# Kernel tuning notes

Hardware: AMD Instinct MI355X
Metric: run time of the kernel (lower is better)

Reference implementation:

```python
import jax, jax.numpy as jnp
import numpy as np

L_F, D_F = 32, 16      # fast window / hop
L_S, D_S = 32, 16      # slow window / hop
H = 32                 # SSM hidden dim
GH = 64                # GRU hidden dim
N_GRU = 4


def setup_inputs() -> dict:
    key = jax.random.key(0)
    ks = jax.random.split(key, 16)
    B, T = 2, 64000
    s = 0.1
    return {
        "x": jax.random.normal(ks[0], (B, T), jnp.float32),
        # slow branch input FC (1 -> GH), stored as (in, out)
        "slow_in_W": jax.random.normal(ks[1], (1, GH), jnp.float32) * s,
        "slow_in_b": jax.random.normal(ks[2], (GH,), jnp.float32) * s,
        # 4 stacked GRU layers, torch gate order [r, z, n], stored (in, 3*GH)
        "gru_Wih": jax.random.normal(ks[3], (N_GRU, GH, 3 * GH), jnp.float32) * s,
        "gru_Whh": jax.random.normal(ks[4], (N_GRU, GH, 3 * GH), jnp.float32) * s,
        "gru_bih": jax.random.normal(ks[5], (N_GRU, 3 * GH), jnp.float32) * s,
        "gru_bhh": jax.random.normal(ks[6], (N_GRU, 3 * GH), jnp.float32) * s,
        # slow branch output FC (GH -> GH)
        "slow_out_W": jax.random.normal(ks[7], (GH, GH), jnp.float32) * s,
        "slow_out_b": jax.random.normal(ks[8], (GH,), jnp.float32) * s,
        # slow_to_ssm (GH -> 2H)
        "s2s_W": jax.random.normal(ks[9], (GH, 2 * H), jnp.float32) * s,
        "s2s_b": jax.random.normal(ks[10], (2 * H,), jnp.float32) * s,
        # fast branch F_IN (1 -> H) and F_OUT (H -> 1)
        "fin_W": jax.random.normal(ks[11], (1, H), jnp.float32) * s,
        "fin_b": jax.random.normal(ks[12], (H,), jnp.float32) * s,
        "fout_W": jax.random.normal(ks[13], (H, 1), jnp.float32) * s,
        "fout_b": jax.random.normal(ks[14], (1,), jnp.float32) * s,
    }


def _forward(x, slow_in_W, slow_in_b, gru_Wih, gru_Whh, gru_bih, gru_bhh,
             slow_out_W, slow_out_b, s2s_W, s2s_b, fin_W, fin_b, fout_W, fout_b):
    B, T = x.shape
    nf = (T - L_F) // D_F + 1   # fast frame count
    ns = (T - L_S) // D_S + 1   # slow frame count
    fidx = jnp.arange(nf)[:, None] * D_F + jnp.arange(L_F)[None, :]  # (nf, L_F)
    sidx = jnp.arange(ns)[:, None] * D_S + jnp.arange(L_S)[None, :]  # (ns, L_S)
    frames = x[:, fidx]                                  # (B, nf, L_F)  == x.unfold

    BS = B * ns
    xs = x[:, sidx].reshape(BS, L_S, 1)
    h = jax.nn.relu(xs @ slow_in_W + slow_in_b)          # (BS, L_S, GH)
    for l in range(N_GRU):
        Whh, bhh = gru_Whh[l], gru_bhh[l]
        xg = h @ gru_Wih[l] + gru_bih[l]                 # (BS, L_S, 3GH)

        def step(hc, xg_t, Whh=Whh, bhh=bhh):
            hg = hc @ Whh + bhh
            r = jax.nn.sigmoid(xg_t[:, :GH] + hg[:, :GH])
            z = jax.nn.sigmoid(xg_t[:, GH:2 * GH] + hg[:, GH:2 * GH])
            n = jnp.tanh(xg_t[:, 2 * GH:] + r * hg[:, 2 * GH:])
            hn = (1.0 - z) * n + z * hc
            return hn, hn

        _, seq = jax.lax.scan(step, jnp.zeros((BS, GH), x.dtype), jnp.swapaxes(xg, 0, 1))
        h = jax.nn.relu(jnp.swapaxes(seq, 0, 1))         # (BS, L_S, GH)
    slow_feat = h[:, -1, :] @ slow_out_W + slow_out_b    # (BS, GH)

    # ---- modulation parameters ----
    eps = (slow_feat @ s2s_W + s2s_b).reshape(B, ns, 2 * H)
    A_s = jax.nn.sigmoid(eps[..., :H])                   # (B, ns, H)
    g_s = eps[..., H:]
    delta = D_S // D_F
    A_flat = jnp.repeat(A_s, delta, axis=1)[:, :nf].reshape(B * nf, H)
    g_flat = jnp.repeat(g_s, delta, axis=1)[:, :nf].reshape(B * nf, H)

    # ---- fast branch: diagonal SSM h_t = A*h_{t-1} + g * F_IN(x_t) ----
    ff = frames.reshape(B * nf, L_F, 1)
    x_emb = (ff @ fin_W + fin_b) * g_flat[:, None, :]    # (B*nf, L_F, H)

    def ssm_step(hc, xt):
        hn = A_flat * hc + xt
        return hn, hn

    _, hall = jax.lax.scan(ssm_step, jnp.zeros((B * nf, H), x.dtype),
                           jnp.swapaxes(x_emb, 0, 1))
    hall = jnp.swapaxes(hall, 0, 1)                      # (B*nf, L_F, H)
    s_hat = (hall @ fout_W + fout_b)[..., 0].reshape(B, nf, L_F)

    # ---- overlap-add (F.fold) ----
    out = jnp.zeros((B, T), x.dtype).at[:, fidx].add(s_hat)
    return out


def reference(x, slow_in_W, slow_in_b, gru_Wih, gru_Whh, gru_bih, gru_bhh,
              slow_out_W, slow_out_b, s2s_W, s2s_b, fin_W, fin_b, fout_W, fout_b):
    return _forward(x, slow_in_W, slow_in_b, gru_Wih, gru_Whh, gru_bih, gru_bhh,
                    slow_out_W, slow_out_b, s2s_W, s2s_b, fin_W, fin_b, fout_W, fout_b)
```

## Files before the change

kernel.cpp:

```cpp
#include <hip/hip_runtime.h>

#define GH 64
#define LS 32
#define HF 32
#define DS 16

#define NLOG2E -1.4426950408889634f
#define P2LOG2E 2.8853900817779268f

typedef short bf16x8 __attribute__((ext_vector_type(8)));
typedef float f32x4 __attribute__((ext_vector_type(4)));

#define MFMA16(a, b, c) __builtin_amdgcn_mfma_f32_16x16x32_bf16(a, b, c, 0, 0, 0)

__device__ __forceinline__ unsigned int f2bf_rne(float f) {
    unsigned int u = __float_as_uint(f);
    return (u + 0x7FFFu + ((u >> 16) & 1u)) >> 16;
}
__device__ __forceinline__ unsigned short f2bf_h(float f) {
    return (unsigned short)((__float_as_uint(f) + 0x8000u) >> 16);
}
__device__ __forceinline__ unsigned int pack_trunc(float v0, float v1) {
    return __builtin_amdgcn_perm(__float_as_uint(v1), __float_as_uint(v0),
                                 0x07060302u);
}
__device__ __forceinline__ bf16x8 as_frag(uint4 u) {
    union { uint4 a; bf16x8 b; } cv; cv.a = u; return cv.b;
}

__device__ __forceinline__ bf16x8 ld_afrag(const unsigned short* slot, int m,
                                           int quad, int half) {
    int b   = half * 4 + quad;
    int idx = (m << 6) + ((b ^ (m & 7)) << 3);
    return as_frag(*reinterpret_cast<const uint4*>(slot + idx));
}

__global__ __launch_bounds__(256) void prep_weights(
    const float* __restrict__ Wih, const float* __restrict__ Whh,
    const float* __restrict__ soW, const float* __restrict__ s2sW,
    unsigned short* __restrict__ wsW)
{
    int idx = blockIdx.x * 256 + threadIdx.x;
    if (idx >= 104 * 1024) return;
    int j = idx & 7, lane = (idx >> 3) & 63, kc = (idx >> 9) & 1, rest = idx >> 10;
    int k = kc * 32 + ((lane >> 4) << 3) + j;
    int c = lane & 15;
    float v;
    if (rest < 96) {
        int jt = rest & 3, mt = rest >> 2;
        int l = mt / 6, mat = mt - l * 6;
        int col = jt * 16 + c;
        const float* W = (mat < 3) ? Wih + (size_t)l * GH * 192
                                   : Whh + (size_t)l * GH * 192;
        int m3 = (mat < 3) ? mat : mat - 3;
        v = W[k * 192 + m3 * 64 + col];
        v *= (m3 == 2) ? P2LOG2E : NLOG2E;
    } else {
        int r2 = rest - 96;
        int jt = r2 & 3, m2 = r2 >> 2;
        int col = jt * 16 + c;
        v = (m2 ? s2sW : soW)[k * 64 + col];
        if (m2 && jt < 2) v *= NLOG2E;
    }
    wsW[idx] = (unsigned short)f2bf_rne(v);
}

__global__ __launch_bounds__(256, 2) void slowfast_fused(
    const float* __restrict__ x,
    const float* __restrict__ siW,  const float* __restrict__ sib,
    const float* __restrict__ bih,  const float* __restrict__ bhh,
    const float* __restrict__ sob,  const float* __restrict__ s2sb,
    const float* __restrict__ finW, const float* __restrict__ finb,
    const float* __restrict__ foutW, const float* __restrict__ foutb,
    const unsigned short* __restrict__ wsW,
    float* __restrict__ out,
    int T, int ns, int BS)
{
    __shared__ __align__(16) unsigned short hseq[LS * 16 * 64];
    __shared__ __align__(16) unsigned short hrec[2 * 16 * 64];
    __shared__ float xs[16 * 33];
    __shared__ float AG[16 * 65];

    const int tid  = threadIdx.x;
    const int lane = tid & 63;
    const int jt   = tid >> 6;
    const int c    = lane & 15;
    const int quad = lane >> 4;
    const int col  = jt * 16 + c;
    const int seqbase = blockIdx.x * 16;
    const uint4* wf = reinterpret_cast<const uint4*>(wsW);

    for (int p = tid; p < 512; p += 256) {
        int seq = p >> 5, t = p & 31;
        int q = seqbase + seq; if (q > BS - 1) q = BS - 1;
        int b  = (q >= ns) ? 1 : 0;
        int si = q - b * ns;
        xs[seq * 33 + t] = x[b * T + si * DS + t];
    }
    __syncthreads();

    {
        int chp = tid & 31;
        int grp = tid >> 5;
        int ch  = chp << 1;
        float w0 = siW[ch], w1 = siW[ch + 1];
        float b0 = sib[ch], b1 = sib[ch + 1];
        #pragma unroll 4
        for (int it = 0; it < 64; ++it) {
            int p = grp + (it << 3);
            int s = p >> 5, t = p & 31;
            float xv = xs[s * 33 + t];
            float v0 = fmaxf(fmaf(xv, w0, b0), 0.0f);
            float v1 = fmaxf(fmaf(xv, w1, b1), 0.0f);
            int idx = (t << 10) + (s << 6) + ((((ch >> 3) ^ (s & 7))) << 3) + (ch & 7);
            *reinterpret_cast<unsigned int*>(&hseq[idx]) = pack_trunc(v0, v1);
        }
    }

    int wIdx[4];
    #pragma unroll
    for (int i = 0; i < 4; ++i) {
        int row = quad * 4 + i;
        wIdx[i] = (row << 6) + ((((col >> 3) ^ (row & 7))) << 3) + (col & 7);
    }

    __syncthreads();

    bf16x8 a0 = ld_afrag(hseq, c, quad, 0);
    bf16x8 a1 = ld_afrag(hseq, c, quad, 1);

    for (int l = 0; l < 4; ++l) {
        bf16x8 BiR[2], BiZ[2], BiN[2], BhR[2], BhZ[2], BhN[2];
        #pragma unroll
        for (int kc = 0; kc < 2; ++kc) {
            int base = (l * 6 * 4 + jt) * 128 + kc * 64 + lane;
            BiR[kc] = as_frag(wf[base]);
            BiZ[kc] = as_frag(wf[base + 512]);
            BiN[kc] = as_frag(wf[base + 1024]);
            BhR[kc] = as_frag(wf[base + 1536]);
            BhZ[kc] = as_frag(wf[base + 2048]);
            BhN[kc] = as_frag(wf[base + 2560]);
        }
        float bRs  = NLOG2E  * (bih[l * 192 + col]      + bhh[l * 192 + col]);
        float bZs  = NLOG2E  * (bih[l * 192 + 64 + col] + bhh[l * 192 + 64 + col]);
        float bNIs = P2LOG2E * bih[l * 192 + 128 + col];
        float bNHs = P2LOG2E * bhh[l * 192 + 128 + col];
        const f32x4 vbR  = (f32x4){bRs,  bRs,  bRs,  bRs};
        const f32x4 vbZ  = (f32x4){bZs,  bZs,  bZs,  bZs};
        const f32x4 vbNI = (f32x4){bNIs, bNIs, bNIs, bNIs};
        const f32x4 vbNH = (f32x4){bNHs, bNHs, bNHs, bNHs};

        float hprev[4] = {0.0f, 0.0f, 0.0f, 0.0f};

        #pragma unroll 2
        for (int t = 0; t < LS; ++t) {
            f32x4 aR  = MFMA16(a0, BiR[0], vbR);
            f32x4 aZ  = MFMA16(a0, BiZ[0], vbZ);
            f32x4 aNI = MFMA16(a0, BiN[0], vbNI);
            aR  = MFMA16(a1, BiR[1], aR);
            aZ  = MFMA16(a1, BiZ[1], aZ);
            aNI = MFMA16(a1, BiN[1], aNI);
            f32x4 aNH = vbNH;
            if (t > 0) {
                const unsigned short* hb = hrec + (((t - 1) & 1) << 10);
                bf16x8 h0 = ld_afrag(hb, c, quad, 0);
                bf16x8 h1 = ld_afrag(hb, c, quad, 1);
                aR  = MFMA16(h0, BhR[0], aR);
                aZ  = MFMA16(h0, BhZ[0], aZ);
                aNH = MFMA16(h0, BhN[0], aNH);
                aR  = MFMA16(h1, BhR[1], aR);
                aZ  = MFMA16(h1, BhZ[1], aZ);
                aNH = MFMA16(h1, BhN[1], aNH);
            }
            unsigned short* wb = hseq + (t << 10);
            unsigned short* wr = hrec + ((t & 1) << 10);
            #pragma unroll
            for (int i = 0; i < 4; ++i) {
                float r  = __builtin_amdgcn_rcpf(1.0f + __builtin_amdgcn_exp2f(aR[i]));
                float z  = __builtin_amdgcn_rcpf(1.0f + __builtin_amdgcn_exp2f(aZ[i]));
                float e  = __builtin_amdgcn_exp2f(fmaf(r, aNH[i], aNI[i]));
                float n  = fmaf(-2.0f, __builtin_amdgcn_rcpf(e + 1.0f), 1.0f);
                float hn = fmaf(z, hprev[i] - n, n);
                hprev[i] = hn;
                wr[wIdx[i]] = f2bf_h(hn);
                wb[wIdx[i]] = f2bf_h(fmaxf(hn, 0.0f));
            }
            const unsigned short* nb = hseq + (((t + 1) & 31) << 10);
            a0 = ld_afrag(nb, c, quad, 0);
            a1 = ld_afrag(nb, c, quad, 1);
            __syncthreads();
        }
    }

    {
        bf16x8 e0 = ld_afrag(hseq + (31 << 10), c, quad, 0);
        bf16x8 e1 = ld_afrag(hseq + (31 << 10), c, quad, 1);
        bf16x8 Bso[2], Bs2[2];
        #pragma unroll
        for (int kc = 0; kc < 2; ++kc) {
            Bso[kc] = as_frag(wf[(96 + jt)  * 128 + kc * 64 + lane]);
            Bs2[kc] = as_frag(wf[(100 + jt) * 128 + kc * 64 + lane]);
        }
        float sb = sob[col];
        f32x4 accS = (f32x4){sb, sb, sb, sb};
        accS = MFMA16(e0, Bso[0], accS);
        accS = MFMA16(e1, Bso[1], accS);
        #pragma unroll
        for (int i = 0; i < 4; ++i)
            hseq[wIdx[i]] = f2bf_h(accS[i]);
        __syncthreads();
        bf16x8 s0 = ld_afrag(hseq, c, quad, 0);
        bf16x8 s1 = ld_afrag(hseq, c, quad, 1);
        float eb = (jt < 2) ? NLOG2E * s2sb[col] : s2sb[col];
        f32x4 accE = (f32x4){eb, eb, eb, eb};
        accE = MFMA16(s0, Bs2[0], accE);
        accE = MFMA16(s1, Bs2[1], accE);
        #pragma unroll
        for (int i = 0; i < 4; ++i) {
            int row = quad * 4 + i;
            float v = accE[i];
            AG[row * 65 + col] = (jt < 2)
                ? __builtin_amdgcn_rcpf(1.0f + __builtin_amdgcn_exp2f(v)) : v;
        }
    }
    __syncthreads();
    {
        int fch = tid & 31;
        float Gfw = finW[fch], Gbw = finb[fch], cFo = foutW[fch], cfb = foutb[0];
        #pragma unroll
        for (int half = 0; half < 2; ++half) {
            int frame = half * 8 + (tid >> 5);
            int q = seqbase + frame;
            if (q < BS) {
                int b  = (q >= ns) ? 1 : 0;
                int fi = q - b * ns;
                float cA = AG[frame * 65 + fch];
                float cG = AG[frame * 65 + 32 + fch];
                float Gf = Gfw * cG;
                float Gb = Gbw * cG;
                float h = 0.0f;
                const float* xrow = xs + frame * 33;
                float* op = out + (size_t)b * T + fi * DS;
                #pragma unroll 1
                for (int t = 0; t < LS; ++t) {
                    h = fmaf(cA, h, fmaf(xrow[t], Gf, Gb));
                    float s = h * cFo;
                    s += __shfl_xor(s, 1);
                    s += __shfl_xor(s, 2);
                    s += __shfl_xor(s, 4);
                    s += __shfl_xor(s, 8);
                    s += __shfl_xor(s, 16);
                    if (fch == 0) atomicAdd(&op[t], s + cfb);
                }
            }
        }
    }
}

extern "C" void kernel_launch(void* const* d_in, const int* in_sizes, int n_in,
                              void* d_out, int out_size, void* d_ws, size_t ws_size,
                              hipStream_t stream)
{
    (void)n_in; (void)ws_size;
    const float* x     = (const float*)d_in[0];
    const float* siW   = (const float*)d_in[1];
    const float* sib   = (const float*)d_in[2];
    const float* Wih   = (const float*)d_in[3];
    const float* Whh   = (const float*)d_in[4];
    const float* bih   = (const float*)d_in[5];
    const float* bhh   = (const float*)d_in[6];
    const float* soW   = (const float*)d_in[7];
    const float* sob   = (const float*)d_in[8];
    const float* s2sW  = (const float*)d_in[9];
    const float* s2sb  = (const float*)d_in[10];
    const float* finW  = (const float*)d_in[11];
    const float* finb  = (const float*)d_in[12];
    const float* foutW = (const float*)d_in[13];
    const float* foutb = (const float*)d_in[14];

    int T  = in_sizes[0] / 2;
    int ns = (T - LS) / DS + 1;
    int BS = 2 * ns;

    unsigned short* wsW = (unsigned short*)d_ws;

    (void)hipMemsetAsync(d_out, 0, (size_t)out_size * sizeof(float), stream);

    prep_weights<<<dim3(416), dim3(256), 0, stream>>>(Wih, Whh, soW, s2sW, wsW);

    slowfast_fused<<<dim3((BS + 15) / 16), dim3(256), 0, stream>>>(
        x, siW, sib, bih, bhh, sob, s2sb, finW, finb, foutW, foutb,
        wsW, (float*)d_out, T, ns, BS);
}
```

Baseline: 171.6 us.

## Wavefront-pipeline GRU layers across warps with two sequence groups per block

The block becomes 1024 threads, with each of 16 waves owning one GRU layer and one column tile. The four layers run as a diagonal wavefront over time steps, and layer outputs pass through small double-buffered LDS rings instead of a full 32-step sequence buffer. Each block handles two 16-sequence groups, so the MFMA chains of two groups interleave. Layer-0 inputs are now built in registers from x, and weights are loaded once per wave. This gives more parallel waves and overlap across layers, at the cost of three extra pipeline steps and a barrier every step across 1024 threads.

```diff
diff --git a/kernel.cpp b/kernel.cpp
--- a/kernel.cpp
+++ b/kernel.cpp
@@ -33,6 +33,27 @@
     int b   = half * 4 + quad;
     int idx = (m << 6) + ((b ^ (m & 7)) << 3);
     return as_frag(*reinterpret_cast<const uint4*>(slot + idx));
+}
+
+__device__ __forceinline__ bf16x8 build_l0(float xv, const float* w, const float* b) {
+    float4 w0 = reinterpret_cast<const float4*>(w)[0];
+    float4 w1 = reinterpret_cast<const float4*>(w)[1];
+    float4 b0 = reinterpret_cast<const float4*>(b)[0];
+    float4 b1 = reinterpret_cast<const float4*>(b)[1];
+    float v0 = fmaxf(fmaf(xv, w0.x, b0.x), 0.0f);
+    float v1 = fmaxf(fmaf(xv, w0.y, b0.y), 0.0f);
+    float v2 = fmaxf(fmaf(xv, w0.z, b0.z), 0.0f);
+    float v3 = fmaxf(fmaf(xv, w0.w, b0.w), 0.0f);
+    float v4 = fmaxf(fmaf(xv, w1.x, b1.x), 0.0f);
+    float v5 = fmaxf(fmaf(xv, w1.y, b1.y), 0.0f);
+    float v6 = fmaxf(fmaf(xv, w1.z, b1.z), 0.0f);
+    float v7 = fmaxf(fmaf(xv, w1.w, b1.w), 0.0f);
+    union { uint4 u; bf16x8 v; } cv;
+    cv.u.x = pack_trunc(v0, v1);
+    cv.u.y = pack_trunc(v2, v3);
+    cv.u.z = pack_trunc(v4, v5);
+    cv.u.w = pack_trunc(v6, v7);
+    return cv.v;
 }
 
 __global__ __launch_bounds__(256) void prep_weights(
@@ -65,7 +86,7 @@
     wsW[idx] = (unsigned short)f2bf_rne(v);
 }
 
-__global__ __launch_bounds__(256, 2) void slowfast_fused(
+__global__ __launch_bounds__(1024, 4) void slowfast_fused(
     const float* __restrict__ x,
     const float* __restrict__ siW,  const float* __restrict__ sib,
     const float* __restrict__ bih,  const float* __restrict__ bhh,
@@ -76,46 +97,52 @@
     float* __restrict__ out,
     int T, int ns, int BS)
 {
-    __shared__ __align__(16) unsigned short hseq[LS * 16 * 64];
-    __shared__ __align__(16) unsigned short hrec[2 * 16 * 64];
-    __shared__ float xs[16 * 33];
-    __shared__ float AG[16 * 65];
+    __shared__ __align__(16) unsigned short ring[2][3][2][1024];
+    __shared__ __align__(16) unsigned short hrec[2][4][2][1024];
+    __shared__ __align__(16) unsigned short h31[2][1024];
+    __shared__ float xs[2][16 * 33];
+    __shared__ float AG[2][16 * 65];
+    __shared__ float swb[128];
 
     const int tid  = threadIdx.x;
     const int lane = tid & 63;
-    const int jt   = tid >> 6;
+    const int wid  = tid >> 6;
+    const int l    = wid >> 2;
+    const int jt   = wid & 3;
     const int c    = lane & 15;
     const int quad = lane >> 4;
     const int col  = jt * 16 + c;
-    const int seqbase = blockIdx.x * 16;
+    const int seqbase = blockIdx.x * 32;
     const uint4* wf = reinterpret_cast<const uint4*>(wsW);
 
-    for (int p = tid; p < 512; p += 256) {
-        int seq = p >> 5, t = p & 31;
-        int q = seqbase + seq; if (q > BS - 1) q = BS - 1;
+    {
+        int s32 = tid >> 5, t = tid & 31;
+        int q = seqbase + s32; if (q > BS - 1) q = BS - 1;
         int b  = (q >= ns) ? 1 : 0;
         int si = q - b * ns;
-        xs[seq * 33 + t] = x[b * T + si * DS + t];
-    }
-    __syncthreads();
-
-    {
-        int chp = tid & 31;
-        int grp = tid >> 5;
-        int ch  = chp << 1;
-        float w0 = siW[ch], w1 = siW[ch + 1];
-        float b0 = sib[ch], b1 = sib[ch + 1];
-        #pragma unroll 4
-        for (int it = 0; it < 64; ++it) {
-            int p = grp + (it << 3);
-            int s = p >> 5, t = p & 31;
-            float xv = xs[s * 33 + t];
-            float v0 = fmaxf(fmaf(xv, w0, b0), 0.0f);
-            float v1 = fmaxf(fmaf(xv, w1, b1), 0.0f);
-            int idx = (t << 10) + (s << 6) + ((((ch >> 3) ^ (s & 7))) << 3) + (ch & 7);
-            *reinterpret_cast<unsigned int*>(&hseq[idx]) = pack_trunc(v0, v1);
-        }
-    }
+        xs[s32 >> 4][(s32 & 15) * 33 + t] = x[b * T + si * DS + t];
+    }
+    if (tid < 64) { swb[tid] = siW[tid]; swb[64 + tid] = sib[tid]; }
+
+    bf16x8 BiR[2], BiZ[2], BiN[2], BhR[2], BhZ[2], BhN[2];
+    #pragma unroll
+    for (int kc = 0; kc < 2; ++kc) {
+        int base = (l * 6 * 4 + jt) * 128 + kc * 64 + lane;
+        BiR[kc] = as_frag(wf[base]);
+        BiZ[kc] = as_frag(wf[base + 512]);
+        BiN[kc] = as_frag(wf[base + 1024]);
+        BhR[kc] = as_frag(wf[base + 1536]);
+        BhZ[kc] = as_frag(wf[base + 2048]);
+        BhN[kc] = as_frag(wf[base + 2560]);
+    }
+    float bRs  = NLOG2E  * (bih[l * 192 + col]      + bhh[l * 192 + col]);
+    float bZs  = NLOG2E  * (bih[l * 192 + 64 + col] + bhh[l * 192 + 64 + col]);
+    float bNIs = P2LOG2E * bih[l * 192 + 128 + col];
+    float bNHs = P2LOG2E * bhh[l * 192 + 128 + col];
+    const f32x4 vbR  = (f32x4){bRs,  bRs,  bRs,  bRs};
+    const f32x4 vbZ  = (f32x4){bZs,  bZs,  bZs,  bZs};
+    const f32x4 vbNI = (f32x4){bNIs, bNIs, bNIs, bNIs};
+    const f32x4 vbNH = (f32x4){bNHs, bNHs, bNHs, bNHs};
 
     int wIdx[4];
     #pragma unroll
@@ -124,93 +151,90 @@
         wIdx[i] = (row << 6) + ((((col >> 3) ^ (row & 7))) << 3) + (col & 7);
     }
 
+    float hprev[2][4] = {{0, 0, 0, 0}, {0, 0, 0, 0}};
+
     __syncthreads();
 
-    bf16x8 a0 = ld_afrag(hseq, c, quad, 0);
-    bf16x8 a1 = ld_afrag(hseq, c, quad, 1);
-
-    for (int l = 0; l < 4; ++l) {
-        bf16x8 BiR[2], BiZ[2], BiN[2], BhR[2], BhZ[2], BhN[2];
+    #pragma unroll 2
+    for (int tau = 0; tau < LS + 3; ++tau) {
+        int t = tau - l;
+        if (t >= 0 && t < LS) {
+            #pragma unroll
+            for (int grp = 0; grp < 2; ++grp) {
+                bf16x8 a0, a1;
+                if (l == 0) {
+                    float xv = xs[grp][c * 33 + t];
+                    a0 = build_l0(xv, &swb[quad * 8],      &swb[64 + quad * 8]);
+                    a1 = build_l0(xv, &swb[32 + quad * 8], &swb[96 + quad * 8]);
+                } else {
+                    const unsigned short* ab = ring[grp][l - 1][t & 1];
+                    a0 = ld_afrag(ab, c, quad, 0);
+                    a1 = ld_afrag(ab, c, quad, 1);
+                }
+                f32x4 aR  = MFMA16(a0, BiR[0], vbR);
+                f32x4 aZ  = MFMA16(a0, BiZ[0], vbZ);
+                f32x4 aNI = MFMA16(a0, BiN[0], vbNI);
+                aR  = MFMA16(a1, BiR[1], aR);
+                aZ  = MFMA16(a1, BiZ[1], aZ);
+                aNI = MFMA16(a1, BiN[1], aNI);
+                f32x4 aNH = vbNH;
+                if (t > 0) {
+                    const unsigned short* hb = hrec[grp][l][(t - 1) & 1];
+                    bf16x8 h0 = ld_afrag(hb, c, quad, 0);
+                    bf16x8 h1 = ld_afrag(hb, c, quad, 1);
+                    aR  = MFMA16(h0, BhR[0], aR);
+                    aZ  = MFMA16(h0, BhZ[0], aZ);
+                    aNH = MFMA16(h0, BhN[0], aNH);
+                    aR  = MFMA16(h1, BhR[1], aR);
+                    aZ  = MFMA16(h1, BhZ[1], aZ);
+                    aNH = MFMA16(h1, BhN[1], aNH);
+                }
+                unsigned short* wr = hrec[grp][l][t & 1];
+                unsigned short* wb = (l < 3) ? ring[grp][l][t & 1] : h31[grp];
+                bool wrelu = (l < 3) | (t == LS - 1);
+                #pragma unroll
+                for (int i = 0; i < 4; ++i) {
+                    float r  = __builtin_amdgcn_rcpf(1.0f + __builtin_amdgcn_exp2f(aR[i]));
+                    float z  = __builtin_amdgcn_rcpf(1.0f + __builtin_amdgcn_exp2f(aZ[i]));
+                    float e  = __builtin_amdgcn_exp2f(fmaf(r, aNH[i], aNI[i]));
+                    float n  = fmaf(-2.0f, __builtin_amdgcn_rcpf(e + 1.0f), 1.0f);
+                    float hn = fmaf(z, hprev[grp][i] - n, n);
+                    hprev[grp][i] = hn;
+                    wr[wIdx[i]] = f2bf_h(hn);
+                    if (wrelu)
+                        wb[wIdx[i]] = f2bf_h(fmaxf(hn, 0.0f));
+                }
+            }
+        }
+        __syncthreads();
+    }
+
+    if (wid < 8) {
+        int grp1 = l;
+        bf16x8 e0 = ld_afrag(h31[grp1], c, quad, 0);
+        bf16x8 e1 = ld_afrag(h31[grp1], c, quad, 1);
+        bf16x8 Bso[2];
         #pragma unroll
-        for (int kc = 0; kc < 2; ++kc) {
-            int base = (l * 6 * 4 + jt) * 128 + kc * 64 + lane;
-            BiR[kc] = as_frag(wf[base]);
-            BiZ[kc] = as_frag(wf[base + 512]);
-            BiN[kc] = as_frag(wf[base + 1024]);
-            BhR[kc] = as_frag(wf[base + 1536]);
-            BhZ[kc] = as_frag(wf[base + 2048]);
-            BhN[kc] = as_frag(wf[base + 2560]);
-        }
-        float bRs  = NLOG2E  * (bih[l * 192 + col]      + bhh[l * 192 + col]);
-        float bZs  = NLOG2E  * (bih[l * 192 + 64 + col] + bhh[l * 192 + 64 + col]);
-        float bNIs = P2LOG2E * bih[l * 192 + 128 + col];
-        float bNHs = P2LOG2E * bhh[l * 192 + 128 + col];
-        const f32x4 vbR  = (f32x4){bRs,  bRs,  bRs,  bRs};
-        const f32x4 vbZ  = (f32x4){bZs,  bZs,  bZs,  bZs};
-        const f32x4 vbNI = (f32x4){bNIs, bNIs, bNIs, bNIs};
-        const f32x4 vbNH = (f32x4){bNHs, bNHs, bNHs, bNHs};
-
-        float hprev[4] = {0.0f, 0.0f, 0.0f, 0.0f};
-
-        #pragma unroll 2
-        for (int t = 0; t < LS; ++t) {
-            f32x4 aR  = MFMA16(a0, BiR[0], vbR);
-            f32x4 aZ  = MFMA16(a0, BiZ[0], vbZ);
-            f32x4 aNI = MFMA16(a0, BiN[0], vbNI);
-            aR  = MFMA16(a1, BiR[1], aR);
-            aZ  = MFMA16(a1, BiZ[1], aZ);
-            aNI = MFMA16(a1, BiN[1], aNI);
-            f32x4 aNH = vbNH;
-            if (t > 0) {
-                const unsigned short* hb = hrec + (((t - 1) & 1) << 10);
-                bf16x8 h0 = ld_afrag(hb, c, quad, 0);
-                bf16x8 h1 = ld_afrag(hb, c, quad, 1);
-                aR  = MFMA16(h0, BhR[0], aR);
-                aZ  = MFMA16(h0, BhZ[0], aZ);
-                aNH = MFMA16(h0, BhN[0], aNH);
-                aR  = MFMA16(h1, BhR[1], aR);
-                aZ  = MFMA16(h1, BhZ[1], aZ);
-                aNH = MFMA16(h1, BhN[1], aNH);
-            }
-            unsigned short* wb = hseq + (t << 10);
-            unsigned short* wr = hrec + ((t & 1) << 10);
-            #pragma unroll
-            for (int i = 0; i < 4; ++i) {
-                float r  = __builtin_amdgcn_rcpf(1.0f + __builtin_amdgcn_exp2f(aR[i]));
-                float z  = __builtin_amdgcn_rcpf(1.0f + __builtin_amdgcn_exp2f(aZ[i]));
-                float e  = __builtin_amdgcn_exp2f(fmaf(r, aNH[i], aNI[i]));
-                float n  = fmaf(-2.0f, __builtin_amdgcn_rcpf(e + 1.0f), 1.0f);
-                float hn = fmaf(z, hprev[i] - n, n);
-                hprev[i] = hn;
-                wr[wIdx[i]] = f2bf_h(hn);
-                wb[wIdx[i]] = f2bf_h(fmaxf(hn, 0.0f));
-            }
-            const unsigned short* nb = hseq + (((t + 1) & 31) << 10);
-            a0 = ld_afrag(nb, c, quad, 0);
-            a1 = ld_afrag(nb, c, quad, 1);
-            __syncthreads();
-        }
-    }
-
-    {
-        bf16x8 e0 = ld_afrag(hseq + (31 << 10), c, quad, 0);
-        bf16x8 e1 = ld_afrag(hseq + (31 << 10), c, quad, 1);
-        bf16x8 Bso[2], Bs2[2];
-        #pragma unroll
-        for (int kc = 0; kc < 2; ++kc) {
-            Bso[kc] = as_frag(wf[(96 + jt)  * 128 + kc * 64 + lane]);
-            Bs2[kc] = as_frag(wf[(100 + jt) * 128 + kc * 64 + lane]);
-        }
+        for (int kc = 0; kc < 2; ++kc)
+            Bso[kc] = as_frag(wf[(96 + jt) * 128 + kc * 64 + lane]);
         float sb = sob[col];
         f32x4 accS = (f32x4){sb, sb, sb, sb};
         accS = MFMA16(e0, Bso[0], accS);
         accS = MFMA16(e1, Bso[1], accS);
+        unsigned short* sf = ring[grp1][0][0];
         #pragma unroll
         for (int i = 0; i < 4; ++i)
-            hseq[wIdx[i]] = f2bf_h(accS[i]);
-        __syncthreads();
-        bf16x8 s0 = ld_afrag(hseq, c, quad, 0);
-        bf16x8 s1 = ld_afrag(hseq, c, quad, 1);
+            sf[wIdx[i]] = f2bf_h(accS[i]);
+    }
+    __syncthreads();
+    if (wid >= 8) {
+        int grp2 = l - 2;
+        bf16x8 s0 = ld_afrag(ring[grp2][0][0], c, quad, 0);
+        bf16x8 s1 = ld_afrag(ring[grp2][0][0], c, quad, 1);
+        bf16x8 Bs2[2];
+        #pragma unroll
+        for (int kc = 0; kc < 2; ++kc)
+            Bs2[kc] = as_frag(wf[(100 + jt) * 128 + kc * 64 + lane]);
         float eb = (jt < 2) ? NLOG2E * s2sb[col] : s2sb[col];
         f32x4 accE = (f32x4){eb, eb, eb, eb};
         accE = MFMA16(s0, Bs2[0], accE);
@@ -219,39 +243,37 @@
         for (int i = 0; i < 4; ++i) {
             int row = quad * 4 + i;
             float v = accE[i];
-            AG[row * 65 + col] = (jt < 2)
+            AG[grp2][row * 65 + col] = (jt < 2)
                 ? __builtin_amdgcn_rcpf(1.0f + __builtin_amdgcn_exp2f(v)) : v;
         }
     }
     __syncthreads();
     {
-        int fch = tid & 31;
-        float Gfw = finW[fch], Gbw = finb[fch], cFo = foutW[fch], cfb = foutb[0];
-        #pragma unroll
-        for (int half = 0; half < 2; ++half) {
-            int frame = half * 8 + (tid >> 5);
-            int q = seqbase + frame;
-            if (q < BS) {
-                int b  = (q >= ns) ? 1 : 0;
-                int fi = q - b * ns;
-                float cA = AG[frame * 65 + fch];
-                float cG = AG[frame * 65 + 32 + fch];
-                float Gf = Gfw * cG;
-                float Gb = Gbw * cG;
-                float h = 0.0f;
-                const float* xrow = xs + frame * 33;
-                float* op = out + (size_t)b * T + fi * DS;
-                #pragma unroll 1
-                for (int t = 0; t < LS; ++t) {
-                    h = fmaf(cA, h, fmaf(xrow[t], Gf, Gb));
-                    float s = h * cFo;
-                    s += __shfl_xor(s, 1);
-                    s += __shfl_xor(s, 2);
-                    s += __shfl_xor(s, 4);
-                    s += __shfl_xor(s, 8);
-                    s += __shfl_xor(s, 16);
-                    if (fch == 0) atomicAdd(&op[t], s + cfb);
-                }
+        int frame = tid >> 5, fch = tid & 31;
+        int grpf = frame >> 4, fr = frame & 15;
+        int q = seqbase + frame;
+        if (q < BS) {
+            int b  = (q >= ns) ? 1 : 0;
+            int fi = q - b * ns;
+            float cA = AG[grpf][fr * 65 + fch];
+            float cG = AG[grpf][fr * 65 + 32 + fch];
+            float Gf = finW[fch] * cG;
+            float Gb = finb[fch] * cG;
+            float cFo = foutW[fch];
+            float cfb = foutb[0];
+            float h = 0.0f;
+            const float* xrow = xs[grpf] + fr * 33;
+            float* op = out + (size_t)b * T + fi * DS;
+            #pragma unroll 1
+            for (int t = 0; t < LS; ++t) {
+                h = fmaf(cA, h, fmaf(xrow[t], Gf, Gb));
+                float s = h * cFo;
+                s += __shfl_xor(s, 1);
+                s += __shfl_xor(s, 2);
+                s += __shfl_xor(s, 4);
+                s += __shfl_xor(s, 8);
+                s += __shfl_xor(s, 16);
+                if (fch == 0) atomicAdd(&op[t], s + cfb);
             }
         }
     }
@@ -288,7 +310,7 @@
 
     prep_weights<<<dim3(416), dim3(256), 0, stream>>>(Wih, Whh, soW, s2sW, wsW);
 
-    slowfast_fused<<<dim3((BS + 15) / 16), dim3(256), 0, stream>>>(
+    slowfast_fused<<<dim3((BS + 31) / 32), dim3(1024), 0, stream>>>(
         x, siW, sib, bih, bhh, sob, s2sb, finW, finb, foutW, foutb,
         wsW, (float*)d_out, T, ns, BS);
 }
```

Result: slower. 177.6 us (+3.5%).

## Double block to 512 threads, splitting GRU gate math across wave pairs

Applied to the files above, without the earlier changes.

Each block now runs 8 waves instead of 4. The two waves that share a column tile each handle half of the four accumulator rows in the GRU elementwise gate math, so the serial transcendental work per wave drops by half. Each wave still issues all of the MFMAs redundantly. The tail stages are split so waves 0-3 do slow_out and waves 4-7 do s2s, and each thread handles one fast-branch frame instead of two. The cost is duplicated MFMA and weight-fragment loads, more register pressure under the new launch bounds, and barriers that now span more waves.

```diff
diff --git a/kernel.cpp b/kernel.cpp
--- a/kernel.cpp
+++ b/kernel.cpp
@@ -65,7 +65,7 @@
     wsW[idx] = (unsigned short)f2bf_rne(v);
 }
 
-__global__ __launch_bounds__(256, 2) void slowfast_fused(
+__global__ __launch_bounds__(512, 4) void slowfast_fused(
     const float* __restrict__ x,
     const float* __restrict__ siW,  const float* __restrict__ sib,
     const float* __restrict__ bih,  const float* __restrict__ bhh,
@@ -83,15 +83,17 @@
 
     const int tid  = threadIdx.x;
     const int lane = tid & 63;
-    const int jt   = tid >> 6;
+    const int wid  = tid >> 6;
+    const int jt   = wid & 3;
+    const int ih   = wid >> 2;
     const int c    = lane & 15;
     const int quad = lane >> 4;
     const int col  = jt * 16 + c;
     const int seqbase = blockIdx.x * 16;
     const uint4* wf = reinterpret_cast<const uint4*>(wsW);
 
-    for (int p = tid; p < 512; p += 256) {
-        int seq = p >> 5, t = p & 31;
+    {
+        int seq = tid >> 5, t = tid & 31;
         int q = seqbase + seq; if (q > BS - 1) q = BS - 1;
         int b  = (q >= ns) ? 1 : 0;
         int si = q - b * ns;
@@ -106,8 +108,8 @@
         float w0 = siW[ch], w1 = siW[ch + 1];
         float b0 = sib[ch], b1 = sib[ch + 1];
         #pragma unroll 4
-        for (int it = 0; it < 64; ++it) {
-            int p = grp + (it << 3);
+        for (int it = 0; it < 32; ++it) {
+            int p = grp + (it << 4);
             int s = p >> 5, t = p & 31;
             float xv = xs[s * 33 + t];
             float v0 = fmaxf(fmaf(xv, w0, b0), 0.0f);
@@ -117,11 +119,11 @@
         }
     }
 
-    int wIdx[4];
+    int wIdx[2];
     #pragma unroll
-    for (int i = 0; i < 4; ++i) {
-        int row = quad * 4 + i;
-        wIdx[i] = (row << 6) + ((((col >> 3) ^ (row & 7))) << 3) + (col & 7);
+    for (int k = 0; k < 2; ++k) {
+        int row = quad * 4 + ih * 2 + k;
+        wIdx[k] = (row << 6) + ((((col >> 3) ^ (row & 7))) << 3) + (col & 7);
     }
 
     __syncthreads();
@@ -150,7 +152,7 @@
         const f32x4 vbNI = (f32x4){bNIs, bNIs, bNIs, bNIs};
         const f32x4 vbNH = (f32x4){bNHs, bNHs, bNHs, bNHs};
 
-        float hprev[4] = {0.0f, 0.0f, 0.0f, 0.0f};
+        float hprev[2] = {0.0f, 0.0f};
 
         #pragma unroll 2
         for (int t = 0; t < LS; ++t) {
@@ -175,15 +177,16 @@
             unsigned short* wb = hseq + (t << 10);
             unsigned short* wr = hrec + ((t & 1) << 10);
             #pragma unroll
-            for (int i = 0; i < 4; ++i) {
-                float r  = __builtin_amdgcn_rcpf(1.0f + __builtin_amdgcn_exp2f(aR[i]));
-                float z  = __builtin_amdgcn_rcpf(1.0f + __builtin_amdgcn_exp2f(aZ[i]));
-                float e  = __builtin_amdgcn_exp2f(fmaf(r, aNH[i], aNI[i]));
+            for (int k = 0; k < 2; ++k) {
+                int ai = ih * 2 + k;
+                float r  = __builtin_amdgcn_rcpf(1.0f + __builtin_amdgcn_exp2f(aR[ai]));
+                float z  = __builtin_amdgcn_rcpf(1.0f + __builtin_amdgcn_exp2f(aZ[ai]));
+                float e  = __builtin_amdgcn_exp2f(fmaf(r, aNH[ai], aNI[ai]));
                 float n  = fmaf(-2.0f, __builtin_amdgcn_rcpf(e + 1.0f), 1.0f);
-                float hn = fmaf(z, hprev[i] - n, n);
-                hprev[i] = hn;
-                wr[wIdx[i]] = f2bf_h(hn);
-                wb[wIdx[i]] = f2bf_h(fmaxf(hn, 0.0f));
+                float hn = fmaf(z, hprev[k] - n, n);
+                hprev[k] = hn;
+                wr[wIdx[k]] = f2bf_h(hn);
+                wb[wIdx[k]] = f2bf_h(fmaxf(hn, 0.0f));
             }
             const unsigned short* nb = hseq + (((t + 1) & 31) << 10);
             a0 = ld_afrag(nb, c, quad, 0);
@@ -192,25 +195,32 @@
         }
     }
 
-    {
+    if (wid < 4) {
         bf16x8 e0 = ld_afrag(hseq + (31 << 10), c, quad, 0);
         bf16x8 e1 = ld_afrag(hseq + (31 << 10), c, quad, 1);
-        bf16x8 Bso[2], Bs2[2];
-        #pragma unroll
-        for (int kc = 0; kc < 2; ++kc) {
-            Bso[kc] = as_frag(wf[(96 + jt)  * 128 + kc * 64 + lane]);
-            Bs2[kc] = as_frag(wf[(100 + jt) * 128 + kc * 64 + lane]);
-        }
+        bf16x8 Bso[2];
+        #pragma unroll
+        for (int kc = 0; kc < 2; ++kc)
+            Bso[kc] = as_frag(wf[(96 + jt) * 128 + kc * 64 + lane]);
         float sb = sob[col];
         f32x4 accS = (f32x4){sb, sb, sb, sb};
         accS = MFMA16(e0, Bso[0], accS);
         accS = MFMA16(e1, Bso[1], accS);
         #pragma unroll
-        for (int i = 0; i < 4; ++i)
-            hseq[wIdx[i]] = f2bf_h(accS[i]);
-        __syncthreads();
+        for (int i = 0; i < 4; ++i) {
+            int row = quad * 4 + i;
+            int idx = (row << 6) + ((((col >> 3) ^ (row & 7))) << 3) + (col & 7);
+            hseq[idx] = f2bf_h(accS[i]);
+        }
+    }
+    __syncthreads();
+    if (wid >= 4) {
         bf16x8 s0 = ld_afrag(hseq, c, quad, 0);
         bf16x8 s1 = ld_afrag(hseq, c, quad, 1);
+        bf16x8 Bs2[2];
+        #pragma unroll
+        for (int kc = 0; kc < 2; ++kc)
+            Bs2[kc] = as_frag(wf[(100 + jt) * 128 + kc * 64 + lane]);
         float eb = (jt < 2) ? NLOG2E * s2sb[col] : s2sb[col];
         f32x4 accE = (f32x4){eb, eb, eb, eb};
         accE = MFMA16(s0, Bs2[0], accE);
@@ -225,33 +235,30 @@
     }
     __syncthreads();
     {
-        int fch = tid & 31;
-        float Gfw = finW[fch], Gbw = finb[fch], cFo = foutW[fch], cfb = foutb[0];
-        #pragma unroll
-        for (int half = 0; half < 2; ++half) {
-            int frame = half * 8 + (tid >> 5);
-            int q = seqbase + frame;
-            if (q < BS) {
-                int b  = (q >= ns) ? 1 : 0;
-                int fi = q - b * ns;
-                float cA = AG[frame * 65 + fch];
-                float cG = AG[frame * 65 + 32 + fch];
-                float Gf = Gfw * cG;
-                float Gb = Gbw * cG;
-                float h = 0.0f;
-                const float* xrow = xs + frame * 33;
-                float* op = out + (size_t)b * T + fi * DS;
-                #pragma unroll 1
-                for (int t = 0; t < LS; ++t) {
-                    h = fmaf(cA, h, fmaf(xrow[t], Gf, Gb));
-                    float s = h * cFo;
-                    s += __shfl_xor(s, 1);
-                    s += __shfl_xor(s, 2);
-                    s += __shfl_xor(s, 4);
-                    s += __shfl_xor(s, 8);
-                    s += __shfl_xor(s, 16);
-                    if (fch == 0) atomicAdd(&op[t], s + cfb);
-                }
+        int frame = tid >> 5, fch = tid & 31;
+        int q = seqbase + frame;
+        if (q < BS) {
+            int b  = (q >= ns) ? 1 : 0;
+            int fi = q - b * ns;
+            float cA = AG[frame * 65 + fch];
+            float cG = AG[frame * 65 + 32 + fch];
+            float Gf = finW[fch] * cG;
+            float Gb = finb[fch] * cG;
+            float cFo = foutW[fch];
+            float cfb = foutb[0];
+            float h = 0.0f;
+            const float* xrow = xs + frame * 33;
+            float* op = out + (size_t)b * T + fi * DS;
+            #pragma unroll 1
+            for (int t = 0; t < LS; ++t) {
+                h = fmaf(cA, h, fmaf(xrow[t], Gf, Gb));
+                float s = h * cFo;
+                s += __shfl_xor(s, 1);
+                s += __shfl_xor(s, 2);
+                s += __shfl_xor(s, 4);
+                s += __shfl_xor(s, 8);
+                s += __shfl_xor(s, 16);
+                if (fch == 0) atomicAdd(&op[t], s + cfb);
             }
         }
     }
@@ -288,7 +295,7 @@
 
     prep_weights<<<dim3(416), dim3(256), 0, stream>>>(Wih, Whh, soW, s2sW, wsW);
 
-    slowfast_fused<<<dim3((BS + 15) / 16), dim3(256), 0, stream>>>(
+    slowfast_fused<<<dim3((BS + 15) / 16), dim3(512), 0, stream>>>(
         x, siW, sib, bih, bhh, sob, s2sb, finW, finb, foutW, foutb,
         wsW, (float*)d_out, T, ns, BS);
 }
```

New measurement: 195.8 us. 14.1% more time.
